# Kernel tuning notes

Measured on AMD Instinct MI355X. Metric: run time of the kernel, lower is better.

Reference implementation:

```python
import jax, jax.numpy as jnp
import numpy as np

N = 63001
F_IN = 512
F_OUT = 256
E = 2_000_000
LRELU_ALPHA = 0.2


def setup_inputs() -> dict:
    key = jax.random.key(0)
    ks = jax.random.split(key, 10)
    x = jax.random.normal(ks[0], (N, F_IN), dtype=jnp.float32)
    values = jax.random.uniform(ks[1], (E,), dtype=jnp.float32)
    edge_index = jax.random.randint(ks[2], (2, E), 0, N, dtype=jnp.int32)
    # learned params: conv1d kernel_size=1 == dense matmuls
    W = jax.random.normal(ks[3], (F_IN, F_OUT), dtype=jnp.float32) * (1.0 / np.sqrt(F_IN))
    a1 = jax.random.normal(ks[4], (F_OUT,), dtype=jnp.float32) * (1.0 / np.sqrt(F_OUT))
    b1 = jnp.zeros((), dtype=jnp.float32)
    a2 = jax.random.normal(ks[5], (F_OUT,), dtype=jnp.float32) * (1.0 / np.sqrt(F_OUT))
    b2 = jnp.zeros((), dtype=jnp.float32)
    b_out = jnp.zeros((F_OUT,), dtype=jnp.float32)
    return {"x": x, "values": values, "edge_index": edge_index,
            "W": W, "a1": a1, "b1": b1, "a2": a2, "b2": b2, "b_out": b_out}


def reference(x, values, edge_index, W, a1, b1, a2, b2, b_out):
    src = edge_index[0]  # row index i of sparse adjacency entry
    dst = edge_index[1]  # col index j

    # conv1d(kernel=1) projections == matmuls
    seq_fts = x @ W                      # [N, F_out]
    f1 = seq_fts @ a1 + b1               # [N]
    f2 = seq_fts @ a2 + b2               # [N]

    # edgewise logits: s_ij * f1_i + s_ij * f2_j  (sparse_add of two masked broadcasts)
    logits = values * (f1[src] + f2[dst])           # [E]
    logits = jax.nn.leaky_relu(logits, LRELU_ALPHA)

    # sparse row-wise softmax over edges grouped by src
    m = jax.ops.segment_max(logits, src, num_segments=N)   # [N]
    p = jnp.exp(logits - m[src])                            # [E]
    denom = jax.ops.segment_sum(p, src, num_segments=N)     # [N]
    coefs = p / denom[src]                                  # [E]

    # SPMM: out_i = sum_j coef_ij * seq_fts_j
    out = jnp.zeros((N, F_OUT), dtype=seq_fts.dtype)
    out = out.at[src].add(coefs[:, None] * seq_fts[dst])

    out = out + b_out                                       # bias_add
    return jax.nn.elu(out)
```

## Files before the change

### kernel.cpp

```cpp
#include <hip/hip_runtime.h>
#include <cstdint>
#include <cstddef>

#define FIN 512
#define FOUT 256
#define LRELU 0.2f

typedef __attribute__((ext_vector_type(8))) short bf16x8;
typedef __attribute__((ext_vector_type(8))) unsigned short u16x8;
typedef __attribute__((ext_vector_type(4))) float f32x4;

__device__ inline ushort f2bf(float f) {
    union { float f; uint32_t u; } c; c.f = f;
    uint32_t u = c.u;
    return (ushort)((u + 0x7FFF + ((u >> 16) & 1)) >> 16);
}
__device__ inline float bf2f(ushort h) {
    union { uint32_t u; float f; } c; c.u = ((uint32_t)h) << 16;
    return c.f;
}

__global__ void prep_wt(const float* __restrict__ W, ushort* __restrict__ WT)
{
    const int idx = blockIdx.x * blockDim.x + threadIdx.x;
    if (idx < FIN * FOUT) {
        const int k = idx >> 8, n = idx & 255;
        WT[(size_t)n * FIN + k] = f2bf(W[(size_t)k * FOUT + n]);
    }
}

#define BM 128
#define BK 64
__global__ __launch_bounds__(512) void gemm_bf16(
    const float* __restrict__ A,
    const ushort* __restrict__ BT,
    ushort* __restrict__ Cbf,
    int M)
{
    __shared__ ushort As[BM * BK];
    __shared__ ushort Bs[FOUT * BK];
    const int t = threadIdx.x;
    const int lane = t & 63, w = t >> 6;
    const int wm = w & 3, wn = w >> 2;
    const int brow = blockIdx.x * BM;

    f32x4 acc[2][8] = {};

    const int ar = t >> 2;
    const int ak = (t & 3) << 4;
    const int bcol = t >> 1;
    const int bkc = (t & 1) * 4;

    for (int k0 = 0; k0 < FIN; k0 += BK) {
        {
            f32x4 v0, v1, v2, v3;
            const int grow = brow + ar;
            if (grow < M) {
                const f32x4* p = (const f32x4*)(A + (size_t)grow * FIN + k0 + ak);
                v0 = __builtin_nontemporal_load(p + 0);
                v1 = __builtin_nontemporal_load(p + 1);
                v2 = __builtin_nontemporal_load(p + 2);
                v3 = __builtin_nontemporal_load(p + 3);
            } else {
                v0 = v1 = v2 = v3 = (f32x4)0.f;
            }
            u16x8 w0, w1;
            w0[0]=f2bf(v0[0]); w0[1]=f2bf(v0[1]); w0[2]=f2bf(v0[2]); w0[3]=f2bf(v0[3]);
            w0[4]=f2bf(v1[0]); w0[5]=f2bf(v1[1]); w0[6]=f2bf(v1[2]); w0[7]=f2bf(v1[3]);
            w1[0]=f2bf(v2[0]); w1[1]=f2bf(v2[1]); w1[2]=f2bf(v2[2]); w1[3]=f2bf(v2[3]);
            w1[4]=f2bf(v3[0]); w1[5]=f2bf(v3[1]); w1[6]=f2bf(v3[2]); w1[7]=f2bf(v3[3]);
            const int c0 = ((ak >> 3) + 0) ^ (ar & 7);
            const int c1 = ((ak >> 3) + 1) ^ (ar & 7);
            *(u16x8*)(&As[ar * BK + (c0 << 3)]) = w0;
            *(u16x8*)(&As[ar * BK + (c1 << 3)]) = w1;
        }
        {
            const ushort* bp = BT + (size_t)bcol * FIN + k0;
#pragma unroll
            for (int j = 0; j < 4; ++j) {
                const int c = bkc + j;
                u16x8 bv = *(const u16x8*)(bp + (c << 3));
                *(u16x8*)(&Bs[bcol * BK + ((c ^ (bcol & 7)) << 3)]) = bv;
            }
        }
        __syncthreads();

#pragma unroll
        for (int kk = 0; kk < 2; ++kk) {
            const int kc = kk * 4 + (lane >> 4);
            bf16x8 af[2], bfr[8];
#pragma unroll
            for (int m = 0; m < 2; ++m) {
                const int row = wm * 32 + m * 16 + (lane & 15);
                af[m] = *(const bf16x8*)(&As[row * BK + ((kc ^ (row & 7)) << 3)]);
            }
#pragma unroll
            for (int n = 0; n < 8; ++n) {
                const int col = wn * 128 + n * 16 + (lane & 15);
                bfr[n] = *(const bf16x8*)(&Bs[col * BK + ((kc ^ (col & 7)) << 3)]);
            }
#pragma unroll
            for (int m = 0; m < 2; ++m)
#pragma unroll
                for (int n = 0; n < 8; ++n)
                    acc[m][n] = __builtin_amdgcn_mfma_f32_16x16x32_bf16(
                        af[m], bfr[n], acc[m][n], 0, 0, 0);
        }
        __syncthreads();
    }

    const int cbase = wn * 128 + (lane & 15);
#pragma unroll
    for (int m = 0; m < 2; ++m) {
#pragma unroll
        for (int reg = 0; reg < 4; ++reg) {
            const int r = brow + wm * 32 + m * 16 + (lane >> 4) * 4 + reg;
            if (r < M) {
#pragma unroll
                for (int n = 0; n < 8; ++n) {
                    Cbf[(size_t)r * FOUT + cbase + n * 16] = f2bf(acc[m][n][reg]);
                }
            }
        }
    }
}

__global__ __launch_bounds__(256) void f1f2_kernel(
    const ushort* __restrict__ seq, const float* __restrict__ a1,
    const float* __restrict__ a2, const float* __restrict__ b1,
    const float* __restrict__ b2, float* __restrict__ f1,
    float* __restrict__ f2, int N)
{
    const int w = threadIdx.x >> 6, lane = threadIdx.x & 63;
    const int row = blockIdx.x * 4 + w;
    if (row >= N) return;
    const ushort4 sv = ((const ushort4*)(seq + (size_t)row * FOUT))[lane];
    const float4 a1v = *(const float4*)(a1 + lane * 4);
    const float4 a2v = *(const float4*)(a2 + lane * 4);
    const float s0 = bf2f(sv.x), s1v = bf2f(sv.y), s2v = bf2f(sv.z), s3 = bf2f(sv.w);
    float s1 = s0 * a1v.x + s1v * a1v.y + s2v * a1v.z + s3 * a1v.w;
    float s2 = s0 * a2v.x + s1v * a2v.y + s2v * a2v.z + s3 * a2v.w;
#pragma unroll
    for (int off = 32; off; off >>= 1) {
        s1 += __shfl_xor(s1, off);
        s2 += __shfl_xor(s2, off);
    }
    if (lane == 0) {
        f1[row] = s1 + b1[0];
        f2[row] = s2 + b2[0];
    }
}

__global__ void pos_kernel(const int* __restrict__ src, int* __restrict__ cnt,
                           int* __restrict__ pos, int E)
{
    int i = (blockIdx.x * blockDim.x + threadIdx.x) * 4;
    if (i + 4 <= E) {
        const int4 s = *(const int4*)(src + i);
        int4 p;
        p.x = atomicAdd(&cnt[s.x], 1);
        p.y = atomicAdd(&cnt[s.y], 1);
        p.z = atomicAdd(&cnt[s.z], 1);
        p.w = atomicAdd(&cnt[s.w], 1);
        *(int4*)(pos + i) = p;
    } else {
        for (; i < E; ++i) pos[i] = atomicAdd(&cnt[src[i]], 1);
    }
}

__global__ __launch_bounds__(1024) void scan_blk(const int* __restrict__ cnt,
                                                 int* __restrict__ btot, int N)
{
    __shared__ int s[1024];
    const int t = threadIdx.x;
    const int idx = blockIdx.x * 1024 + t;
    s[t] = (idx < N) ? cnt[idx] : 0;
    __syncthreads();
    for (int off = 512; off; off >>= 1) {
        if (t < off) s[t] += s[t + off];
        __syncthreads();
    }
    if (t == 0) btot[blockIdx.x] = s[0];
}

__global__ __launch_bounds__(64) void scan_top(const int* __restrict__ btot,
                                               int* __restrict__ boff, int nb)
{
    const int t = threadIdx.x;
    const int mine = (t < nb) ? btot[t] : 0;
    int v = mine;
#pragma unroll
    for (int off = 1; off < 64; off <<= 1) {
        const int u = __shfl_up(v, off);
        if (t >= off) v += u;
    }
    if (t < nb) boff[t] = v - mine;
}

__global__ __launch_bounds__(1024) void scan_out(const int* __restrict__ cnt,
                                                 const int* __restrict__ boff,
                                                 int* __restrict__ rowoff, int N)
{
    __shared__ int s[1024];
    const int t = threadIdx.x;
    const int b = blockIdx.x;
    const int idx = b * 1024 + t;
    const int v = (idx < N) ? cnt[idx] : 0;
    s[t] = v;
    __syncthreads();
    for (int off = 1; off < 1024; off <<= 1) {
        const int u = (t >= off) ? s[t - off] : 0;
        __syncthreads();
        s[t] += u;
        __syncthreads();
    }
    if (idx < N)     rowoff[idx] = boff[b] + s[t] - v;
    if (idx == N - 1) rowoff[N]  = boff[b] + s[t];
}

__global__ void scatter_p(const int* __restrict__ src, const int* __restrict__ dst,
                          const float* __restrict__ values, const int* __restrict__ pos,
                          const float* __restrict__ f1, const float* __restrict__ f2,
                          const int* __restrict__ row_off,
                          unsigned long long* __restrict__ pd, int E)
{
    const int i = blockIdx.x * blockDim.x + threadIdx.x;
    if (i < E) {
        const int s = src[i];
        const int d = dst[i];
        float lg = values[i] * (f1[s] + f2[d]);
        lg = (lg > 0.f) ? lg : LRELU * lg;
        const float p = __expf(lg);
        union { float f; uint32_t u; } pu; pu.f = p;
        const unsigned long long rec = (unsigned long long)pu.u |
                                       ((unsigned long long)(uint32_t)d << 32);
        __builtin_nontemporal_store(rec, &pd[row_off[s] + pos[i]]);
    }
}

__global__ __launch_bounds__(256) void spmm_kernel(
    const ushort* __restrict__ seq, const unsigned long long* __restrict__ pd,
    const int* __restrict__ row_off, const float* __restrict__ b_out,
    float* __restrict__ out, int N)
{
    const int w = threadIdx.x >> 6, lane = threadIdx.x & 63;
    const int row = blockIdx.x * 4 + w;
    if (row >= N) return;
    const int start = row_off[row], end = row_off[row + 1];

    float4 a0 = make_float4(0.f,0.f,0.f,0.f), a1 = a0, a2 = a0, a3 = a0;
    float den0 = 0.f, den1 = 0.f, den2 = 0.f, den3 = 0.f;
    int t = start;
    for (; t + 4 <= end; t += 4) {
        const unsigned long long q0 = __builtin_nontemporal_load(&pd[t]);
        const unsigned long long q1 = __builtin_nontemporal_load(&pd[t + 1]);
        const unsigned long long q2 = __builtin_nontemporal_load(&pd[t + 2]);
        const unsigned long long q3 = __builtin_nontemporal_load(&pd[t + 3]);
        const float p0 = __uint_as_float((uint32_t)q0), p1 = __uint_as_float((uint32_t)q1);
        const float p2 = __uint_as_float((uint32_t)q2), p3 = __uint_as_float((uint32_t)q3);
        const int d0 = (int)(q0 >> 32), d1 = (int)(q1 >> 32);
        const int d2 = (int)(q2 >> 32), d3 = (int)(q3 >> 32);
        const ushort4 s0 = ((const ushort4*)(seq + (size_t)d0 * FOUT))[lane];
        const ushort4 s1 = ((const ushort4*)(seq + (size_t)d1 * FOUT))[lane];
        const ushort4 s2 = ((const ushort4*)(seq + (size_t)d2 * FOUT))[lane];
        const ushort4 s3 = ((const ushort4*)(seq + (size_t)d3 * FOUT))[lane];
        den0 += p0; den1 += p1; den2 += p2; den3 += p3;
        a0.x += p0 * bf2f(s0.x); a0.y += p0 * bf2f(s0.y);
        a0.z += p0 * bf2f(s0.z); a0.w += p0 * bf2f(s0.w);
        a1.x += p1 * bf2f(s1.x); a1.y += p1 * bf2f(s1.y);
        a1.z += p1 * bf2f(s1.z); a1.w += p1 * bf2f(s1.w);
        a2.x += p2 * bf2f(s2.x); a2.y += p2 * bf2f(s2.y);
        a2.z += p2 * bf2f(s2.z); a2.w += p2 * bf2f(s2.w);
        a3.x += p3 * bf2f(s3.x); a3.y += p3 * bf2f(s3.y);
        a3.z += p3 * bf2f(s3.z); a3.w += p3 * bf2f(s3.w);
    }
    for (; t < end; ++t) {
        const unsigned long long q0 = __builtin_nontemporal_load(&pd[t]);
        const float p0 = __uint_as_float((uint32_t)q0);
        const int d0 = (int)(q0 >> 32);
        const ushort4 s0 = ((const ushort4*)(seq + (size_t)d0 * FOUT))[lane];
        den0 += p0;
        a0.x += p0 * bf2f(s0.x); a0.y += p0 * bf2f(s0.y);
        a0.z += p0 * bf2f(s0.z); a0.w += p0 * bf2f(s0.w);
    }
    const float denom = (den0 + den1) + (den2 + den3);
    const float inv = (end > start) ? 1.f / denom : 0.f;
    const float4 bo = *(const float4*)(b_out + lane * 4);
    f32x4 o;
    o[0] = ((a0.x + a1.x) + (a2.x + a3.x)) * inv + bo.x;
    o[1] = ((a0.y + a1.y) + (a2.y + a3.y)) * inv + bo.y;
    o[2] = ((a0.z + a1.z) + (a2.z + a3.z)) * inv + bo.z;
    o[3] = ((a0.w + a1.w) + (a2.w + a3.w)) * inv + bo.w;
    o[0] = (o[0] > 0.f) ? o[0] : expm1f(o[0]);
    o[1] = (o[1] > 0.f) ? o[1] : expm1f(o[1]);
    o[2] = (o[2] > 0.f) ? o[2] : expm1f(o[2]);
    o[3] = (o[3] > 0.f) ? o[3] : expm1f(o[3]);
    __builtin_nontemporal_store(o, (f32x4*)(out + (size_t)row * FOUT + lane * 4));
}

extern "C" void kernel_launch(void* const* d_in, const int* in_sizes, int n_in,
                              void* d_out, int out_size, void* d_ws, size_t ws_size,
                              hipStream_t stream)
{
    const float* x      = (const float*)d_in[0];
    const float* values = (const float*)d_in[1];
    const int*   ei     = (const int*)d_in[2];
    const float* W      = (const float*)d_in[3];
    const float* a1     = (const float*)d_in[4];
    const float* b1     = (const float*)d_in[5];
    const float* a2     = (const float*)d_in[6];
    const float* b2     = (const float*)d_in[7];
    const float* b_out  = (const float*)d_in[8];
    float* out = (float*)d_out;

    const int N = in_sizes[0] / FIN;
    const int E = in_sizes[1];
    const int* src = ei;
    const int* dst = ei + E;

    auto alignup = [](size_t v) { return (v + 255) & ~(size_t)255; };
    char* ws = (char*)d_ws;
    size_t off = 0;
    ushort* seqbf = (ushort*)(ws + off); off = alignup(off + (size_t)N * FOUT * 2);
    ushort* WT    = (ushort*)(ws + off); off = alignup(off + (size_t)FIN * FOUT * 2);
    float*  f1    = (float*)(ws + off);  off = alignup(off + (size_t)N * 4);
    float*  f2    = (float*)(ws + off);  off = alignup(off + (size_t)N * 4);
    int*    cnt   = (int*)(ws + off);    off = alignup(off + (size_t)N * 4);
    int*    rowoff= (int*)(ws + off);    off = alignup(off + (size_t)(N + 1) * 4);
    int*    btot  = (int*)(ws + off);    off = alignup(off + (size_t)64 * 4);
    int*    boff  = (int*)(ws + off);    off = alignup(off + (size_t)64 * 4);
    int*    pos   = (int*)(ws + off);    off = alignup(off + (size_t)E * 4);
    unsigned long long* pd = (unsigned long long*)(ws + off); off = alignup(off + (size_t)E * 8);
    (void)ws_size;

    const int nb = (N + 1023) / 1024;

    hipMemsetAsync(cnt, 0, (size_t)N * 4, stream);

    pos_kernel<<<(E / 4 + 255) / 256, 256, 0, stream>>>(src, cnt, pos, E);
    scan_blk<<<nb, 1024, 0, stream>>>(cnt, btot, N);
    scan_top<<<1, 64, 0, stream>>>(btot, boff, nb);
    scan_out<<<nb, 1024, 0, stream>>>(cnt, boff, rowoff, N);

    prep_wt<<<(FIN * FOUT + 255) / 256, 256, 0, stream>>>(W, WT);
    gemm_bf16<<<(N + BM - 1) / BM, 512, 0, stream>>>(x, WT, seqbf, N);
    f1f2_kernel<<<(N + 3) / 4, 256, 0, stream>>>(seqbf, a1, a2, b1, b2, f1, f2, N);

    scatter_p<<<(E + 255) / 256, 256, 0, stream>>>(src, dst, values, pos, f1, f2,
                                                   rowoff, pd, E);

    spmm_kernel<<<(N + 3) / 4, 256, 0, stream>>>(seqbf, pd, rowoff, b_out, out, N);
}
```

Before: 392.0 us.

## Bucket edges by destination range within rows and fuse f1/f2 into GEMM epilogue

Edges in each source row are now sub-bucketed by the high bits of the destination (8 buckets), so the CSR stores neighbours in roughly ascending destination order. The aim is better cache locality for the bf16 feature gathers in the SpMM. The f1/f2 attention projections are computed in the GEMM epilogue from the fp32 accumulators, which removes a separate pass over seq_fts. In exchange the count and offset arrays grow eightfold, scan_top becomes a 1024-thread scan, and the SpMM loads of pd drop the nontemporal hint.

```diff
diff --git a/kernel.cpp b/kernel.cpp
--- a/kernel.cpp
+++ b/kernel.cpp
@@ -5,6 +5,8 @@
 #define FIN 512
 #define FOUT 256
 #define LRELU 0.2f
+#define NBKT 8
+#define BSH 13
 
 typedef __attribute__((ext_vector_type(8))) short bf16x8;
 typedef __attribute__((ext_vector_type(8))) unsigned short u16x8;
@@ -35,10 +37,15 @@
     const float* __restrict__ A,
     const ushort* __restrict__ BT,
     ushort* __restrict__ Cbf,
+    const float* __restrict__ a1, const float* __restrict__ a2,
+    const float* __restrict__ b1, const float* __restrict__ b2,
+    float* __restrict__ f1, float* __restrict__ f2,
     int M)
 {
     __shared__ ushort As[BM * BK];
     __shared__ ushort Bs[FOUT * BK];
+    __shared__ float f1s[BM][2];
+    __shared__ float f2s[BM][2];
     const int t = threadIdx.x;
     const int lane = t & 63, w = t >> 6;
     const int wm = w & 3, wn = w >> 2;
@@ -109,72 +116,77 @@
         __syncthreads();
     }
 
+    float a1c[8], a2c[8];
+#pragma unroll
+    for (int n = 0; n < 8; ++n) {
+        const int col = wn * 128 + n * 16 + (lane & 15);
+        a1c[n] = a1[col];
+        a2c[n] = a2[col];
+    }
     const int cbase = wn * 128 + (lane & 15);
 #pragma unroll
     for (int m = 0; m < 2; ++m) {
 #pragma unroll
         for (int reg = 0; reg < 4; ++reg) {
-            const int r = brow + wm * 32 + m * 16 + (lane >> 4) * 4 + reg;
+            const int rloc = wm * 32 + m * 16 + (lane >> 4) * 4 + reg;
+            const int r = brow + rloc;
+            float p1 = 0.f, p2 = 0.f;
+#pragma unroll
+            for (int n = 0; n < 8; ++n) {
+                p1 += acc[m][n][reg] * a1c[n];
+                p2 += acc[m][n][reg] * a2c[n];
+            }
+#pragma unroll
+            for (int off = 1; off < 16; off <<= 1) {
+                p1 += __shfl_xor(p1, off);
+                p2 += __shfl_xor(p2, off);
+            }
+            if ((lane & 15) == 0) {
+                f1s[rloc][wn] = p1;
+                f2s[rloc][wn] = p2;
+            }
             if (r < M) {
 #pragma unroll
-                for (int n = 0; n < 8; ++n) {
+                for (int n = 0; n < 8; ++n)
                     Cbf[(size_t)r * FOUT + cbase + n * 16] = f2bf(acc[m][n][reg]);
-                }
-            }
-        }
-    }
-}
-
-__global__ __launch_bounds__(256) void f1f2_kernel(
-    const ushort* __restrict__ seq, const float* __restrict__ a1,
-    const float* __restrict__ a2, const float* __restrict__ b1,
-    const float* __restrict__ b2, float* __restrict__ f1,
-    float* __restrict__ f2, int N)
-{
-    const int w = threadIdx.x >> 6, lane = threadIdx.x & 63;
-    const int row = blockIdx.x * 4 + w;
-    if (row >= N) return;
-    const ushort4 sv = ((const ushort4*)(seq + (size_t)row * FOUT))[lane];
-    const float4 a1v = *(const float4*)(a1 + lane * 4);
-    const float4 a2v = *(const float4*)(a2 + lane * 4);
-    const float s0 = bf2f(sv.x), s1v = bf2f(sv.y), s2v = bf2f(sv.z), s3 = bf2f(sv.w);
-    float s1 = s0 * a1v.x + s1v * a1v.y + s2v * a1v.z + s3 * a1v.w;
-    float s2 = s0 * a2v.x + s1v * a2v.y + s2v * a2v.z + s3 * a2v.w;
-#pragma unroll
-    for (int off = 32; off; off >>= 1) {
-        s1 += __shfl_xor(s1, off);
-        s2 += __shfl_xor(s2, off);
-    }
-    if (lane == 0) {
-        f1[row] = s1 + b1[0];
-        f2[row] = s2 + b2[0];
-    }
-}
-
-__global__ void pos_kernel(const int* __restrict__ src, int* __restrict__ cnt,
-                           int* __restrict__ pos, int E)
+            }
+        }
+    }
+    __syncthreads();
+    if (t < BM) {
+        const int r = brow + t;
+        if (r < M) {
+            f1[r] = f1s[t][0] + f1s[t][1] + b1[0];
+            f2[r] = f2s[t][0] + f2s[t][1] + b2[0];
+        }
+    }
+}
+
+__global__ void pos_kernel(const int* __restrict__ src, const int* __restrict__ dst,
+                           int* __restrict__ cnt, int* __restrict__ pos, int E)
 {
     int i = (blockIdx.x * blockDim.x + threadIdx.x) * 4;
     if (i + 4 <= E) {
         const int4 s = *(const int4*)(src + i);
+        const int4 d = *(const int4*)(dst + i);
         int4 p;
-        p.x = atomicAdd(&cnt[s.x], 1);
-        p.y = atomicAdd(&cnt[s.y], 1);
-        p.z = atomicAdd(&cnt[s.z], 1);
-        p.w = atomicAdd(&cnt[s.w], 1);
+        p.x = atomicAdd(&cnt[s.x * NBKT + (d.x >> BSH)], 1);
+        p.y = atomicAdd(&cnt[s.y * NBKT + (d.y >> BSH)], 1);
+        p.z = atomicAdd(&cnt[s.z * NBKT + (d.z >> BSH)], 1);
+        p.w = atomicAdd(&cnt[s.w * NBKT + (d.w >> BSH)], 1);
         *(int4*)(pos + i) = p;
     } else {
-        for (; i < E; ++i) pos[i] = atomicAdd(&cnt[src[i]], 1);
+        for (; i < E; ++i) pos[i] = atomicAdd(&cnt[src[i] * NBKT + (dst[i] >> BSH)], 1);
     }
 }
 
 __global__ __launch_bounds__(1024) void scan_blk(const int* __restrict__ cnt,
-                                                 int* __restrict__ btot, int N)
+                                                 int* __restrict__ btot, int K)
 {
     __shared__ int s[1024];
     const int t = threadIdx.x;
     const int idx = blockIdx.x * 1024 + t;
-    s[t] = (idx < N) ? cnt[idx] : 0;
+    s[t] = (idx < K) ? cnt[idx] : 0;
     __syncthreads();
     for (int off = 512; off; off >>= 1) {
         if (t < off) s[t] += s[t + off];
@@ -183,29 +195,32 @@
     if (t == 0) btot[blockIdx.x] = s[0];
 }
 
-__global__ __launch_bounds__(64) void scan_top(const int* __restrict__ btot,
-                                               int* __restrict__ boff, int nb)
-{
+__global__ __launch_bounds__(1024) void scan_top(const int* __restrict__ btot,
+                                                 int* __restrict__ boff, int nb)
+{
+    __shared__ int s[1024];
     const int t = threadIdx.x;
     const int mine = (t < nb) ? btot[t] : 0;
-    int v = mine;
-#pragma unroll
-    for (int off = 1; off < 64; off <<= 1) {
-        const int u = __shfl_up(v, off);
-        if (t >= off) v += u;
-    }
-    if (t < nb) boff[t] = v - mine;
+    s[t] = mine;
+    __syncthreads();
+    for (int off = 1; off < 1024; off <<= 1) {
+        const int u = (t >= off) ? s[t - off] : 0;
+        __syncthreads();
+        s[t] += u;
+        __syncthreads();
+    }
+    if (t < nb) boff[t] = s[t] - mine;
 }
 
 __global__ __launch_bounds__(1024) void scan_out(const int* __restrict__ cnt,
                                                  const int* __restrict__ boff,
-                                                 int* __restrict__ rowoff, int N)
+                                                 int* __restrict__ koff, int K)
 {
     __shared__ int s[1024];
     const int t = threadIdx.x;
     const int b = blockIdx.x;
     const int idx = b * 1024 + t;
-    const int v = (idx < N) ? cnt[idx] : 0;
+    const int v = (idx < K) ? cnt[idx] : 0;
     s[t] = v;
     __syncthreads();
     for (int off = 1; off < 1024; off <<= 1) {
@@ -214,14 +229,14 @@
         s[t] += u;
         __syncthreads();
     }
-    if (idx < N)     rowoff[idx] = boff[b] + s[t] - v;
-    if (idx == N - 1) rowoff[N]  = boff[b] + s[t];
+    if (idx < K)      koff[idx] = boff[b] + s[t] - v;
+    if (idx == K - 1) koff[K]   = boff[b] + s[t];
 }
 
 __global__ void scatter_p(const int* __restrict__ src, const int* __restrict__ dst,
                           const float* __restrict__ values, const int* __restrict__ pos,
                           const float* __restrict__ f1, const float* __restrict__ f2,
-                          const int* __restrict__ row_off,
+                          const int* __restrict__ koff,
                           unsigned long long* __restrict__ pd, int E)
 {
     const int i = blockIdx.x * blockDim.x + threadIdx.x;
@@ -234,28 +249,28 @@
         union { float f; uint32_t u; } pu; pu.f = p;
         const unsigned long long rec = (unsigned long long)pu.u |
                                        ((unsigned long long)(uint32_t)d << 32);
-        __builtin_nontemporal_store(rec, &pd[row_off[s] + pos[i]]);
+        __builtin_nontemporal_store(rec, &pd[koff[s * NBKT + (d >> BSH)] + pos[i]]);
     }
 }
 
 __global__ __launch_bounds__(256) void spmm_kernel(
     const ushort* __restrict__ seq, const unsigned long long* __restrict__ pd,
-    const int* __restrict__ row_off, const float* __restrict__ b_out,
+    const int* __restrict__ koff, const float* __restrict__ b_out,
     float* __restrict__ out, int N)
 {
     const int w = threadIdx.x >> 6, lane = threadIdx.x & 63;
     const int row = blockIdx.x * 4 + w;
     if (row >= N) return;
-    const int start = row_off[row], end = row_off[row + 1];
+    const int start = koff[row * NBKT], end = koff[(row + 1) * NBKT];
 
     float4 a0 = make_float4(0.f,0.f,0.f,0.f), a1 = a0, a2 = a0, a3 = a0;
     float den0 = 0.f, den1 = 0.f, den2 = 0.f, den3 = 0.f;
     int t = start;
     for (; t + 4 <= end; t += 4) {
-        const unsigned long long q0 = __builtin_nontemporal_load(&pd[t]);
-        const unsigned long long q1 = __builtin_nontemporal_load(&pd[t + 1]);
-        const unsigned long long q2 = __builtin_nontemporal_load(&pd[t + 2]);
-        const unsigned long long q3 = __builtin_nontemporal_load(&pd[t + 3]);
+        const unsigned long long q0 = pd[t];
+        const unsigned long long q1 = pd[t + 1];
+        const unsigned long long q2 = pd[t + 2];
+        const unsigned long long q3 = pd[t + 3];
         const float p0 = __uint_as_float((uint32_t)q0), p1 = __uint_as_float((uint32_t)q1);
         const float p2 = __uint_as_float((uint32_t)q2), p3 = __uint_as_float((uint32_t)q3);
         const int d0 = (int)(q0 >> 32), d1 = (int)(q1 >> 32);
@@ -275,7 +290,7 @@
         a3.z += p3 * bf2f(s3.z); a3.w += p3 * bf2f(s3.w);
     }
     for (; t < end; ++t) {
-        const unsigned long long q0 = __builtin_nontemporal_load(&pd[t]);
+        const unsigned long long q0 = pd[t];
         const float p0 = __uint_as_float((uint32_t)q0);
         const int d0 = (int)(q0 >> 32);
         const ushort4 s0 = ((const ushort4*)(seq + (size_t)d0 * FOUT))[lane];
@@ -317,6 +332,7 @@
     const int E = in_sizes[1];
     const int* src = ei;
     const int* dst = ei + E;
+    const int K = N * NBKT;
 
     auto alignup = [](size_t v) { return (v + 255) & ~(size_t)255; };
     char* ws = (char*)d_ws;
@@ -325,29 +341,29 @@
     ushort* WT    = (ushort*)(ws + off); off = alignup(off + (size_t)FIN * FOUT * 2);
     float*  f1    = (float*)(ws + off);  off = alignup(off + (size_t)N * 4);
     float*  f2    = (float*)(ws + off);  off = alignup(off + (size_t)N * 4);
-    int*    cnt   = (int*)(ws + off);    off = alignup(off + (size_t)N * 4);
-    int*    rowoff= (int*)(ws + off);    off = alignup(off + (size_t)(N + 1) * 4);
-    int*    btot  = (int*)(ws + off);    off = alignup(off + (size_t)64 * 4);
-    int*    boff  = (int*)(ws + off);    off = alignup(off + (size_t)64 * 4);
+    int*    cnt   = (int*)(ws + off);    off = alignup(off + (size_t)K * 4);
+    int*    koff  = (int*)(ws + off);    off = alignup(off + (size_t)(K + 1) * 4);
+    int*    btot  = (int*)(ws + off);    off = alignup(off + (size_t)1024 * 4);
+    int*    boff  = (int*)(ws + off);    off = alignup(off + (size_t)1024 * 4);
     int*    pos   = (int*)(ws + off);    off = alignup(off + (size_t)E * 4);
     unsigned long long* pd = (unsigned long long*)(ws + off); off = alignup(off + (size_t)E * 8);
     (void)ws_size;
 
-    const int nb = (N + 1023) / 1024;
-
-    hipMemsetAsync(cnt, 0, (size_t)N * 4, stream);
-
-    pos_kernel<<<(E / 4 + 255) / 256, 256, 0, stream>>>(src, cnt, pos, E);
-    scan_blk<<<nb, 1024, 0, stream>>>(cnt, btot, N);
-    scan_top<<<1, 64, 0, stream>>>(btot, boff, nb);
-    scan_out<<<nb, 1024, 0, stream>>>(cnt, boff, rowoff, N);
+    const int nbk = (K + 1023) / 1024;
+
+    hipMemsetAsync(cnt, 0, (size_t)K * 4, stream);
+
+    pos_kernel<<<(E / 4 + 255) / 256, 256, 0, stream>>>(src, dst, cnt, pos, E);
+    scan_blk<<<nbk, 1024, 0, stream>>>(cnt, btot, K);
+    scan_top<<<1, 1024, 0, stream>>>(btot, boff, nbk);
+    scan_out<<<nbk, 1024, 0, stream>>>(cnt, boff, koff, K);
 
     prep_wt<<<(FIN * FOUT + 255) / 256, 256, 0, stream>>>(W, WT);
-    gemm_bf16<<<(N + BM - 1) / BM, 512, 0, stream>>>(x, WT, seqbf, N);
-    f1f2_kernel<<<(N + 3) / 4, 256, 0, stream>>>(seqbf, a1, a2, b1, b2, f1, f2, N);
+    gemm_bf16<<<(N + BM - 1) / BM, 512, 0, stream>>>(x, WT, seqbf, a1, a2, b1, b2,
+                                                     f1, f2, N);
 
     scatter_p<<<(E + 255) / 256, 256, 0, stream>>>(src, dst, values, pos, f1, f2,
-                                                   rowoff, pd, E);
-
-    spmm_kernel<<<(N + 3) / 4, 256, 0, stream>>>(seqbf, pd, rowoff, b_out, out, N);
-}
+                                                   koff, pd, E);
+
+    spmm_kernel<<<(N + 3) / 4, 256, 0, stream>>>(seqbf, pd, koff, b_out, out, N);
+}
```

Result: faster. 357.5 us (-8.8%).
